# Performance work log

Measured on AMD Instinct MI355X. Metric: run time of the kernel, lower is better.

Reference implementation:

```python
import jax, jax.numpy as jnp
import numpy as np

B, L, C, D = 32, 4096, 64, 128
TOPK = max(1, int(L * 0.5))


def setup_inputs() -> dict:
    key = jax.random.key(0)
    ks = jax.random.split(key, 9)
    s = lambda k, sh: jax.random.normal(k, sh, dtype=jnp.float32) * 0.02
    return {
        "x": jax.random.normal(ks[0], (B, L, C), dtype=jnp.float32),
        "score_w": s(ks[1], (C,)),
        "score_b": jnp.zeros((), jnp.float32),
        "sparse_w": s(ks[2], (C, D)),
        "sparse_b": jnp.zeros((D,), jnp.float32),
        "full_w": s(ks[3], (C, D)),
        "full_b": jnp.zeros((D,), jnp.float32),
        "ln_g": jnp.ones((D,), jnp.float32),
        "ln_b": jnp.zeros((D,), jnp.float32),
    }


def _layernorm(h, g, b, eps=1e-5):
    mu = jnp.mean(h, axis=-1, keepdims=True)
    var = jnp.mean(jnp.square(h - mu), axis=-1, keepdims=True)
    return (h - mu) * jax.lax.rsqrt(var + eps) * g + b


def reference(x, score_w, score_b, sparse_w, sparse_b, full_w, full_b, ln_g, ln_b):
    # scores: (B, L)
    scores = jnp.einsum("blc,c->bl", x, score_w) + score_b
    _, idx = jax.lax.top_k(scores, TOPK)              # (B, K)
    sparse_x = jnp.take_along_axis(x, idx[:, :, None], axis=1)  # (B, K, C)
    sparse_feat = jax.nn.gelu(jnp.einsum("bkc,cd->bkd", sparse_x, sparse_w) + sparse_b, approximate=False)
    sparse_agg = jnp.mean(sparse_feat, axis=1, keepdims=True)   # (B, 1, D)
    full_feat = jnp.einsum("blc,cd->bld", x, full_w) + full_b   # (B, L, D)
    out = _layernorm(full_feat + sparse_agg, ln_g, ln_b)
    return out
```

## Files before the change

### kernel.cpp

```cpp
#include <hip/hip_runtime.h>
#include <math.h>

static constexpr int PB = 32;
static constexpr int PL = 4096;
static constexpr int PC = 64;
static constexpr int PD = 128;
static constexpr int PK = 2048;

typedef __attribute__((ext_vector_type(8))) short bf16x8;
typedef __attribute__((ext_vector_type(4))) float f32x4;

#define MFMA_BF16(A, B, C) __builtin_amdgcn_mfma_f32_16x16x32_bf16(A, B, C, 0, 0, 0)

__device__ inline short f2bf(float f) {
  unsigned u = __float_as_uint(f);
  u += 0x7FFFu + ((u >> 16) & 1u);
  return (short)(u >> 16);
}

__global__ __launch_bounds__(256) void scores_kernel(
    const float* __restrict__ x, const float* __restrict__ score_w,
    const float* __restrict__ score_b, const float* __restrict__ sparse_w,
    const float* __restrict__ full_w, float* __restrict__ scores,
    short* __restrict__ xbf, unsigned* __restrict__ wtfg) {
  int tid = threadIdx.x;

  if (blockIdx.x < 2) {
    const float* w = (blockIdx.x == 0) ? sparse_w : full_w;
    unsigned* dst = wtfg + blockIdx.x * 4096;
    for (int i = tid; i < 4096; i += 256) {
      int d = i & 127, cp = i >> 7, c = cp * 2;
      float va = w[(size_t)c * PD + d];
      float vb = w[(size_t)(c + 1) * PD + d];
      unsigned lo = (unsigned short)f2bf(va);
      unsigned hi = (unsigned short)f2bf(vb);
      int t = d >> 4, dl = d & 15, h = c >> 5, cq = (c >> 3) & 3, jp = (c & 7) >> 1;
      dst[(((t * 2 + h) * 4 + cq) * 16 + dl) * 4 + jp] = lo | (hi << 16);
    }
  }

  int r  = tid >> 4;
  int c4 = tid & 15;
  int row = blockIdx.x * 16 + r;
  float4 xv = *(const float4*)(x + (size_t)row * PC + c4 * 4);
  float4 wv = *(const float4*)(score_w + c4 * 4);

  short4 xbv;
  xbv.x = f2bf(xv.x); xbv.y = f2bf(xv.y); xbv.z = f2bf(xv.z); xbv.w = f2bf(xv.w);
  *(short4*)(xbf + (size_t)row * PC + c4 * 4) = xbv;

  float v = xv.x * wv.x + xv.y * wv.y + xv.z * wv.z + xv.w * wv.w;
  #pragma unroll
  for (int off = 1; off < 16; off <<= 1) v += __shfl_xor(v, off);
  if (c4 == 0) scores[row] = v + score_b[0];
}

__global__ __launch_bounds__(256) void select_kernel(
    const float* __restrict__ scores, int* __restrict__ selidx,
    float* __restrict__ agg) {
  __shared__ unsigned hist4[4 * 256];
  __shared__ unsigned sbuf[257];
  __shared__ unsigned wsum[4];
  __shared__ unsigned sh_prefix, sh_need;

  int tid = threadIdx.x;
  int lane = tid & 63;
  int wid  = tid >> 6;
  int b = blockIdx.x;
  const float* sc = scores + (size_t)b * PL;

  unsigned k[16];
  #pragma unroll
  for (int q = 0; q < 4; ++q) {
    float4 f = *(const float4*)(sc + tid * 16 + q * 4);
    unsigned u0 = __float_as_uint(f.x), u1 = __float_as_uint(f.y);
    unsigned u2 = __float_as_uint(f.z), u3 = __float_as_uint(f.w);
    k[q * 4 + 0] = (u0 & 0x80000000u) ? ~u0 : (u0 | 0x80000000u);
    k[q * 4 + 1] = (u1 & 0x80000000u) ? ~u1 : (u1 | 0x80000000u);
    k[q * 4 + 2] = (u2 & 0x80000000u) ? ~u2 : (u2 | 0x80000000u);
    k[q * 4 + 3] = (u3 & 0x80000000u) ? ~u3 : (u3 | 0x80000000u);
  }

  if (tid == 0) { sh_prefix = 0u; sh_need = (unsigned)PK; sbuf[256] = 0u; }
  if (tid < PD) agg[(size_t)b * PD + tid] = 0.f;

  for (int r = 3; r >= 0; --r) {
    int shift = r * 8;
    #pragma unroll
    for (int w = 0; w < 4; ++w) hist4[w * 256 + tid] = 0u;
    __syncthreads();
    unsigned prefix = sh_prefix;
    unsigned need   = sh_need;
    unsigned maskAbove = (r == 3) ? 0u : (~0u << (shift + 8));
    unsigned* myhist = &hist4[wid * 256];
    #pragma unroll
    for (int j = 0; j < 16; ++j) {
      if ((k[j] & maskAbove) == prefix)
        atomicAdd(&myhist[(k[j] >> shift) & 255u], 1u);
    }
    __syncthreads();
    unsigned v = hist4[tid] + hist4[256 + tid] + hist4[512 + tid] + hist4[768 + tid];
    #pragma unroll
    for (int off = 1; off < 64; off <<= 1) {
      unsigned t = __shfl_down(v, off);
      if (lane + off < 64) v += t;
    }
    if (lane == 0) wsum[wid] = v;
    __syncthreads();
    unsigned add = 0;
    #pragma unroll
    for (int w = 0; w < 4; ++w) if (w > wid) add += wsum[w];
    sbuf[tid] = v + add;
    __syncthreads();
    if (sbuf[tid] >= need && sbuf[tid + 1] < need) {
      sh_prefix = prefix | ((unsigned)tid << shift);
      sh_need = need - sbuf[tid + 1];
    }
  }
  __syncthreads();
  unsigned T = sh_prefix;
  unsigned needEq = sh_need;

  int base = tid * 16;
  unsigned ceq = 0;
  #pragma unroll
  for (int j = 0; j < 16; ++j) ceq += (k[j] == T);

  unsigned v1 = ceq;
  #pragma unroll
  for (int off = 1; off < 64; off <<= 1) {
    unsigned t = __shfl_up(v1, off);
    if (lane >= off) v1 += t;
  }
  if (lane == 63) wsum[wid] = v1;
  __syncthreads();
  unsigned add1 = 0;
  #pragma unroll
  for (int w = 0; w < 4; ++w) if (w < wid) add1 += wsum[w];
  unsigned eqbase = v1 + add1 - ceq;
  __syncthreads();

  unsigned csel = 0, eqr = eqbase;
  #pragma unroll
  for (int j = 0; j < 16; ++j) {
    if (k[j] > T) csel++;
    else if (k[j] == T) { if (eqr < needEq) csel++; eqr++; }
  }
  unsigned v2 = csel;
  #pragma unroll
  for (int off = 1; off < 64; off <<= 1) {
    unsigned t = __shfl_up(v2, off);
    if (lane >= off) v2 += t;
  }
  if (lane == 63) wsum[wid] = v2;
  __syncthreads();
  unsigned add2 = 0;
  #pragma unroll
  for (int w = 0; w < 4; ++w) if (w < wid) add2 += wsum[w];
  unsigned pos = v2 + add2 - csel;

  eqr = eqbase;
  int* outp = selidx + (size_t)b * PK;
  #pragma unroll
  for (int j = 0; j < 16; ++j) {
    bool sel;
    if (k[j] > T) sel = true;
    else if (k[j] == T) { sel = (eqr < needEq); eqr++; }
    else sel = false;
    if (sel) outp[pos++] = base + j;
  }
}

__device__ inline void stage_wtf(const unsigned* __restrict__ g, unsigned* lds, int tid) {
  #pragma unroll
  for (int q = 0; q < 4; ++q) {
    uint4 v = *(const uint4*)(g + q * 1024 + tid * 4);
    *(uint4*)(lds + q * 1024 + tid * 4) = v;
  }
}

__global__ __launch_bounds__(256, 3) void sparse_kernel(
    const short* __restrict__ xbf, const unsigned* __restrict__ wtfg,
    const float* __restrict__ sparse_b, const int* __restrict__ selidx,
    float* __restrict__ agg) {
  __shared__ unsigned WTf[4096];
  __shared__ float red[PD];
  int tid = threadIdx.x;
  stage_wtf(wtfg, WTf, tid);
  if (tid < PD) red[tid] = 0.f;
  __syncthreads();

  int lane = tid & 63, wid = tid >> 6;
  int ln = lane & 15, quad = lane >> 4;
  int b  = blockIdx.x >> 4;
  int rb = blockIdx.x & 15;
  int j0 = rb * 128 + wid * 32 + ln;
  const int* sel = selidx + (size_t)b * PK;
  int r0 = sel[j0], r1 = sel[j0 + 16];

  const short* xb = xbf + (size_t)b * PL * PC;
  const short* p0 = xb + (size_t)r0 * PC + quad * 8;
  const short* p1 = xb + (size_t)r1 * PC + quad * 8;
  bf16x8 a00 = *(const bf16x8*)p0, a01 = *(const bf16x8*)(p0 + 32);
  bf16x8 a10 = *(const bf16x8*)p1, a11 = *(const bf16x8*)(p1 + 32);

  f32x4 acc0[8], acc1[8];
  #pragma unroll
  for (int t = 0; t < 8; ++t) { acc0[t] = (f32x4){0.f,0.f,0.f,0.f}; acc1[t] = (f32x4){0.f,0.f,0.f,0.f}; }

  const short* wb = (const short*)WTf + lane * 8;
  #pragma unroll
  for (int t = 0; t < 8; ++t) {
    bf16x8 b0 = *(const bf16x8*)(wb + (2 * t) * 512);
    bf16x8 b1 = *(const bf16x8*)(wb + (2 * t + 1) * 512);
    acc0[t] = MFMA_BF16(a00, b0, acc0[t]);
    acc0[t] = MFMA_BF16(a01, b1, acc0[t]);
    acc1[t] = MFMA_BF16(a10, b0, acc1[t]);
    acc1[t] = MFMA_BF16(a11, b1, acc1[t]);
  }

  #pragma unroll
  for (int t = 0; t < 8; ++t) {
    float bias = sparse_b[t * 16 + ln];
    float s = 0.f;
    #pragma unroll
    for (int i = 0; i < 4; ++i) {
      float v0 = acc0[t][i] + bias;
      s += 0.5f * v0 * (1.0f + erff(v0 * 0.70710678118654752f));
      float v1 = acc1[t][i] + bias;
      s += 0.5f * v1 * (1.0f + erff(v1 * 0.70710678118654752f));
    }
    s += __shfl_xor(s, 16);
    s += __shfl_xor(s, 32);
    if (quad == 0) atomicAdd(&red[t * 16 + ln], s);
  }
  __syncthreads();
  if (tid < PD) atomicAdd(&agg[(size_t)b * PD + tid], red[tid]);
}

__global__ __launch_bounds__(256, 3) void full_ln_kernel(
    const short* __restrict__ xbf, const unsigned* __restrict__ wtfg,
    const float* __restrict__ full_b, const float* __restrict__ ln_g,
    const float* __restrict__ ln_b, const float* __restrict__ agg,
    float* __restrict__ out) {
  __shared__ unsigned WTf[4096];
  int tid = threadIdx.x;
  stage_wtf(wtfg, WTf, tid);
  __syncthreads();

  int lane = tid & 63, wid = tid >> 6;
  int ln = lane & 15, quad = lane >> 4;
  int rowbase = blockIdx.x * 128 + wid * 32;
  int b = rowbase >> 12;

  const float invK = 1.0f / (float)PK;
  float bias[8], gg[8], bb[8];
  #pragma unroll
  for (int t = 0; t < 8; ++t) {
    int d = t * 16 + ln;
    bias[t] = full_b[d] + agg[(size_t)b * PD + d] * invK;
    gg[t] = ln_g[d];
    bb[t] = ln_b[d];
  }

  const short* p0 = xbf + (size_t)(rowbase + ln) * PC + quad * 8;
  const short* p1 = xbf + (size_t)(rowbase + 16 + ln) * PC + quad * 8;
  bf16x8 a00 = *(const bf16x8*)p0, a01 = *(const bf16x8*)(p0 + 32);
  bf16x8 a10 = *(const bf16x8*)p1, a11 = *(const bf16x8*)(p1 + 32);

  f32x4 acc0[8], acc1[8];
  #pragma unroll
  for (int t = 0; t < 8; ++t) { acc0[t] = (f32x4){0.f,0.f,0.f,0.f}; acc1[t] = (f32x4){0.f,0.f,0.f,0.f}; }

  const short* wb = (const short*)WTf + lane * 8;
  #pragma unroll
  for (int t = 0; t < 8; ++t) {
    bf16x8 b0 = *(const bf16x8*)(wb + (2 * t) * 512);
    bf16x8 b1 = *(const bf16x8*)(wb + (2 * t + 1) * 512);
    acc0[t] = MFMA_BF16(a00, b0, acc0[t]);
    acc0[t] = MFMA_BF16(a01, b1, acc0[t]);
    acc1[t] = MFMA_BF16(a10, b0, acc1[t]);
    acc1[t] = MFMA_BF16(a11, b1, acc1[t]);
  }

#define LN_EPILOGUE(ACC, GOFF) do {                                          \
    float s_[4] = {0.f,0.f,0.f,0.f}, ss_[4] = {0.f,0.f,0.f,0.f};             \
    _Pragma("unroll")                                                        \
    for (int t = 0; t < 8; ++t) {                                            \
      _Pragma("unroll")                                                      \
      for (int i = 0; i < 4; ++i) {                                          \
        float h_ = ACC[t][i] + bias[t];                                      \
        ACC[t][i] = h_;                                                      \
        s_[i] += h_; ss_[i] += h_ * h_;                                      \
      }                                                                      \
    }                                                                        \
    _Pragma("unroll")                                                        \
    for (int i = 0; i < 4; ++i) {                                            \
      _Pragma("unroll")                                                      \
      for (int off = 1; off < 16; off <<= 1) {                               \
        s_[i]  += __shfl_xor(s_[i], off);                                    \
        ss_[i] += __shfl_xor(ss_[i], off);                                   \
      }                                                                      \
    }                                                                        \
    _Pragma("unroll")                                                        \
    for (int i = 0; i < 4; ++i) {                                            \
      float mu_  = s_[i] * (1.0f / 128.0f);                                  \
      float var_ = ss_[i] * (1.0f / 128.0f) - mu_ * mu_;                     \
      float inv_ = rsqrtf(var_ + 1e-5f);                                     \
      int r_ = rowbase + (GOFF) + quad * 4 + i;                              \
      float* op_ = out + (size_t)r_ * PD + ln;                               \
      _Pragma("unroll")                                                      \
      for (int t = 0; t < 8; ++t)                                            \
        op_[t * 16] = (ACC[t][i] - mu_) * inv_ * gg[t] + bb[t];              \
    }                                                                        \
  } while (0)

  LN_EPILOGUE(acc0, 0);
  LN_EPILOGUE(acc1, 16);
#undef LN_EPILOGUE
}

extern "C" void kernel_launch(void* const* d_in, const int* in_sizes, int n_in,
                              void* d_out, int out_size, void* d_ws, size_t ws_size,
                              hipStream_t stream) {
  const float* x        = (const float*)d_in[0];
  const float* score_w  = (const float*)d_in[1];
  const float* score_b  = (const float*)d_in[2];
  const float* sparse_w = (const float*)d_in[3];
  const float* sparse_b = (const float*)d_in[4];
  const float* full_w   = (const float*)d_in[5];
  const float* full_b   = (const float*)d_in[6];
  const float* ln_g     = (const float*)d_in[7];
  const float* ln_b     = (const float*)d_in[8];
  float* out = (float*)d_out;

  char* ws = (char*)d_ws;
  float*    scores = (float*)ws;
  int*      selidx = (int*)(ws + (512 << 10));
  float*    agg    = (float*)(ws + (768 << 10));
  unsigned* wtfg   = (unsigned*)(ws + (784 << 10));
  short*    xbf    = (short*)(ws + (816 << 10));

  scores_kernel<<<PB * PL / 16, 256, 0, stream>>>(x, score_w, score_b, sparse_w,
                                                  full_w, scores, xbf, wtfg);
  select_kernel<<<PB, 256, 0, stream>>>(scores, selidx, agg);
  sparse_kernel<<<PB * (PK / 128), 256, 0, stream>>>(xbf, wtfg, sparse_b, selidx, agg);
  full_ln_kernel<<<PB * PL / 128, 256, 0, stream>>>(xbf, wtfg + 4096, full_b,
                                                    ln_g, ln_b, agg, out);
}
```

Baseline: 131.8 us.

## Fuse score computation and top-k selection via last-block-done atomic counter

Merges the scores kernel and the select kernel into one launch. Each block now processes 128 rows, and the last block to finish for each batch runs the radix-select, detected through a per-batch atomic counter that a memset zeroes before launch. The histogram rows are padded to a stride of 264 to reduce LDS bank conflicts. This removes one kernel launch and its gap, but adds a memset, threadfences, and a serialized select tail inside the fused kernel.

```diff
diff --git a/kernel.cpp b/kernel.cpp
--- a/kernel.cpp
+++ b/kernel.cpp
@@ -12,22 +12,34 @@
 
 #define MFMA_BF16(A, B, C) __builtin_amdgcn_mfma_f32_16x16x32_bf16(A, B, C, 0, 0, 0)
 
+static constexpr int HSTR = 264;
+
 __device__ inline short f2bf(float f) {
   unsigned u = __float_as_uint(f);
   u += 0x7FFFu + ((u >> 16) & 1u);
   return (short)(u >> 16);
 }
 
-__global__ __launch_bounds__(256) void scores_kernel(
+__global__ __launch_bounds__(256) void scores_select_kernel(
     const float* __restrict__ x, const float* __restrict__ score_w,
     const float* __restrict__ score_b, const float* __restrict__ sparse_w,
     const float* __restrict__ full_w, float* __restrict__ scores,
-    short* __restrict__ xbf, unsigned* __restrict__ wtfg) {
+    short* __restrict__ xbf, unsigned* __restrict__ wtfg,
+    int* __restrict__ selidx, float* __restrict__ agg,
+    unsigned* __restrict__ done) {
+  __shared__ unsigned hist4[4 * HSTR];
+  __shared__ unsigned sbuf[257];
+  __shared__ unsigned wsum[4];
+  __shared__ unsigned sh_prefix, sh_need;
+  __shared__ int sh_last;
+
   int tid = threadIdx.x;
-
-  if (blockIdx.x < 2) {
-    const float* w = (blockIdx.x == 0) ? sparse_w : full_w;
-    unsigned* dst = wtfg + blockIdx.x * 4096;
+  int blk = blockIdx.x;
+  int b = blk >> 5;
+
+  if (blk < 2) {
+    const float* w = (blk == 0) ? sparse_w : full_w;
+    unsigned* dst = wtfg + blk * 4096;
     for (int i = tid; i < 4096; i += 256) {
       int d = i & 127, cp = i >> 7, c = cp * 2;
       float va = w[(size_t)c * PD + d];
@@ -41,32 +53,29 @@
 
   int r  = tid >> 4;
   int c4 = tid & 15;
-  int row = blockIdx.x * 16 + r;
-  float4 xv = *(const float4*)(x + (size_t)row * PC + c4 * 4);
   float4 wv = *(const float4*)(score_w + c4 * 4);
-
-  short4 xbv;
-  xbv.x = f2bf(xv.x); xbv.y = f2bf(xv.y); xbv.z = f2bf(xv.z); xbv.w = f2bf(xv.w);
-  *(short4*)(xbf + (size_t)row * PC + c4 * 4) = xbv;
-
-  float v = xv.x * wv.x + xv.y * wv.y + xv.z * wv.z + xv.w * wv.w;
-  #pragma unroll
-  for (int off = 1; off < 16; off <<= 1) v += __shfl_xor(v, off);
-  if (c4 == 0) scores[row] = v + score_b[0];
-}
-
-__global__ __launch_bounds__(256) void select_kernel(
-    const float* __restrict__ scores, int* __restrict__ selidx,
-    float* __restrict__ agg) {
-  __shared__ unsigned hist4[4 * 256];
-  __shared__ unsigned sbuf[257];
-  __shared__ unsigned wsum[4];
-  __shared__ unsigned sh_prefix, sh_need;
-
-  int tid = threadIdx.x;
+  float sb0 = score_b[0];
+  #pragma unroll
+  for (int it = 0; it < 8; ++it) {
+    int row = blk * 128 + it * 16 + r;
+    float4 xv = *(const float4*)(x + (size_t)row * PC + c4 * 4);
+    short4 xbv;
+    xbv.x = f2bf(xv.x); xbv.y = f2bf(xv.y); xbv.z = f2bf(xv.z); xbv.w = f2bf(xv.w);
+    *(short4*)(xbf + (size_t)row * PC + c4 * 4) = xbv;
+    float v = xv.x * wv.x + xv.y * wv.y + xv.z * wv.z + xv.w * wv.w;
+    #pragma unroll
+    for (int off = 1; off < 16; off <<= 1) v += __shfl_xor(v, off);
+    if (c4 == 0) scores[row] = v + sb0;
+  }
+
+  __threadfence();
+  if (tid == 0) sh_last = (atomicAdd(&done[b], 1u) == 31u);
+  __syncthreads();
+  if (!sh_last) return;
+  __threadfence();
+
   int lane = tid & 63;
   int wid  = tid >> 6;
-  int b = blockIdx.x;
   const float* sc = scores + (size_t)b * PL;
 
   unsigned k[16];
@@ -84,22 +93,22 @@
   if (tid == 0) { sh_prefix = 0u; sh_need = (unsigned)PK; sbuf[256] = 0u; }
   if (tid < PD) agg[(size_t)b * PD + tid] = 0.f;
 
-  for (int r = 3; r >= 0; --r) {
-    int shift = r * 8;
-    #pragma unroll
-    for (int w = 0; w < 4; ++w) hist4[w * 256 + tid] = 0u;
+  for (int rr = 3; rr >= 0; --rr) {
+    int shift = rr * 8;
+    #pragma unroll
+    for (int w = 0; w < 4; ++w) hist4[w * HSTR + tid] = 0u;
     __syncthreads();
     unsigned prefix = sh_prefix;
     unsigned need   = sh_need;
-    unsigned maskAbove = (r == 3) ? 0u : (~0u << (shift + 8));
-    unsigned* myhist = &hist4[wid * 256];
+    unsigned maskAbove = (rr == 3) ? 0u : (~0u << (shift + 8));
+    unsigned* myhist = &hist4[wid * HSTR];
     #pragma unroll
     for (int j = 0; j < 16; ++j) {
       if ((k[j] & maskAbove) == prefix)
         atomicAdd(&myhist[(k[j] >> shift) & 255u], 1u);
     }
     __syncthreads();
-    unsigned v = hist4[tid] + hist4[256 + tid] + hist4[512 + tid] + hist4[768 + tid];
+    unsigned v = hist4[tid] + hist4[HSTR + tid] + hist4[2 * HSTR + tid] + hist4[3 * HSTR + tid];
     #pragma unroll
     for (int off = 1; off < 64; off <<= 1) {
       unsigned t = __shfl_down(v, off);
@@ -339,11 +348,12 @@
   int*      selidx = (int*)(ws + (512 << 10));
   float*    agg    = (float*)(ws + (768 << 10));
   unsigned* wtfg   = (unsigned*)(ws + (784 << 10));
-  short*    xbf    = (short*)(ws + (816 << 10));
-
-  scores_kernel<<<PB * PL / 16, 256, 0, stream>>>(x, score_w, score_b, sparse_w,
-                                                  full_w, scores, xbf, wtfg);
-  select_kernel<<<PB, 256, 0, stream>>>(scores, selidx, agg);
+  unsigned* done   = (unsigned*)(ws + (816 << 10));
+  short*    xbf    = (short*)(ws + (817 << 10));
+
+  hipMemsetAsync(done, 0, PB * sizeof(unsigned), stream);
+  scores_select_kernel<<<PB * PL / 128, 256, 0, stream>>>(
+      x, score_w, score_b, sparse_w, full_w, scores, xbf, wtfg, selidx, agg, done);
   sparse_kernel<<<PB * (PK / 128), 256, 0, stream>>>(xbf, wtfg, sparse_b, selidx, agg);
   full_ln_kernel<<<PB * PL / 128, 256, 0, stream>>>(xbf, wtfg + 4096, full_b,
                                                     ln_g, ln_b, agg, out);
```

After: 238.1 us. +80.6%, slower.

## Fuse top-k selection into sparse kernel, recomputing radix select per block

Applied to the files above, without the earlier changes.

Removes the separate select kernel and its selidx global buffer. Each sparse block now redundantly runs the radix top-k threshold search over its batch's 4096 scores and keeps only the 128 selected indices it owns in LDS. The agg zeroing moves into the scores kernel. This saves one launch and the serial 32-block select stage, but the selection work is repeated 16 times per batch and the LDS footprint per block grows.

```diff
diff --git a/kernel.cpp b/kernel.cpp
--- a/kernel.cpp
+++ b/kernel.cpp
@@ -22,7 +22,8 @@
     const float* __restrict__ x, const float* __restrict__ score_w,
     const float* __restrict__ score_b, const float* __restrict__ sparse_w,
     const float* __restrict__ full_w, float* __restrict__ scores,
-    short* __restrict__ xbf, unsigned* __restrict__ wtfg) {
+    short* __restrict__ xbf, unsigned* __restrict__ wtfg,
+    float* __restrict__ agg) {
   int tid = threadIdx.x;
 
   if (blockIdx.x < 2) {
@@ -38,6 +39,8 @@
       dst[(((t * 2 + h) * 4 + cq) * 16 + dl) * 4 + jp] = lo | (hi << 16);
     }
   }
+  if ((blockIdx.x & 255) == 0 && tid < PD)
+    agg[(size_t)(blockIdx.x >> 8) * PD + tid] = 0.f;
 
   int r  = tid >> 4;
   int c4 = tid & 15;
@@ -55,18 +58,33 @@
   if (c4 == 0) scores[row] = v + score_b[0];
 }
 
-__global__ __launch_bounds__(256) void select_kernel(
-    const float* __restrict__ scores, int* __restrict__ selidx,
+__device__ inline void stage_wtf(const unsigned* __restrict__ g, unsigned* lds, int tid) {
+  #pragma unroll
+  for (int q = 0; q < 4; ++q) {
+    uint4 v = *(const uint4*)(g + q * 1024 + tid * 4);
+    *(uint4*)(lds + q * 1024 + tid * 4) = v;
+  }
+}
+
+__global__ __launch_bounds__(256, 3) void sparse_kernel(
+    const short* __restrict__ xbf, const unsigned* __restrict__ wtfg,
+    const float* __restrict__ sparse_b, const float* __restrict__ scores,
     float* __restrict__ agg) {
+  __shared__ unsigned WTf[4096];
+  __shared__ float red[PD];
   __shared__ unsigned hist4[4 * 256];
   __shared__ unsigned sbuf[257];
   __shared__ unsigned wsum[4];
   __shared__ unsigned sh_prefix, sh_need;
+  __shared__ int sel_l[128];
 
   int tid = threadIdx.x;
-  int lane = tid & 63;
-  int wid  = tid >> 6;
-  int b = blockIdx.x;
+  stage_wtf(wtfg, WTf, tid);
+  if (tid < PD) red[tid] = 0.f;
+
+  int lane = tid & 63, wid = tid >> 6;
+  int b  = blockIdx.x >> 4;
+  int rb = blockIdx.x & 15;
   const float* sc = scores + (size_t)b * PL;
 
   unsigned k[16];
@@ -80,18 +98,16 @@
     k[q * 4 + 2] = (u2 & 0x80000000u) ? ~u2 : (u2 | 0x80000000u);
     k[q * 4 + 3] = (u3 & 0x80000000u) ? ~u3 : (u3 | 0x80000000u);
   }
-
   if (tid == 0) { sh_prefix = 0u; sh_need = (unsigned)PK; sbuf[256] = 0u; }
-  if (tid < PD) agg[(size_t)b * PD + tid] = 0.f;
-
-  for (int r = 3; r >= 0; --r) {
-    int shift = r * 8;
+
+  for (int rr = 3; rr >= 0; --rr) {
+    int shift = rr * 8;
     #pragma unroll
     for (int w = 0; w < 4; ++w) hist4[w * 256 + tid] = 0u;
     __syncthreads();
     unsigned prefix = sh_prefix;
     unsigned need   = sh_need;
-    unsigned maskAbove = (r == 3) ? 0u : (~0u << (shift + 8));
+    unsigned maskAbove = (rr == 3) ? 0u : (~0u << (shift + 8));
     unsigned* myhist = &hist4[wid * 256];
     #pragma unroll
     for (int j = 0; j < 16; ++j) {
@@ -159,44 +175,24 @@
   for (int w = 0; w < 4; ++w) if (w < wid) add2 += wsum[w];
   unsigned pos = v2 + add2 - csel;
 
+  int lo = rb * 128;
   eqr = eqbase;
-  int* outp = selidx + (size_t)b * PK;
   #pragma unroll
   for (int j = 0; j < 16; ++j) {
     bool sel;
     if (k[j] > T) sel = true;
     else if (k[j] == T) { sel = (eqr < needEq); eqr++; }
     else sel = false;
-    if (sel) outp[pos++] = base + j;
-  }
-}
-
-__device__ inline void stage_wtf(const unsigned* __restrict__ g, unsigned* lds, int tid) {
-  #pragma unroll
-  for (int q = 0; q < 4; ++q) {
-    uint4 v = *(const uint4*)(g + q * 1024 + tid * 4);
-    *(uint4*)(lds + q * 1024 + tid * 4) = v;
-  }
-}
-
-__global__ __launch_bounds__(256, 3) void sparse_kernel(
-    const short* __restrict__ xbf, const unsigned* __restrict__ wtfg,
-    const float* __restrict__ sparse_b, const int* __restrict__ selidx,
-    float* __restrict__ agg) {
-  __shared__ unsigned WTf[4096];
-  __shared__ float red[PD];
-  int tid = threadIdx.x;
-  stage_wtf(wtfg, WTf, tid);
-  if (tid < PD) red[tid] = 0.f;
-  __syncthreads();
-
-  int lane = tid & 63, wid = tid >> 6;
+    if (sel) {
+      int p = (int)pos++;
+      if (p >= lo && p < lo + 128) sel_l[p - lo] = base + j;
+    }
+  }
+  __syncthreads();
+
   int ln = lane & 15, quad = lane >> 4;
-  int b  = blockIdx.x >> 4;
-  int rb = blockIdx.x & 15;
-  int j0 = rb * 128 + wid * 32 + ln;
-  const int* sel = selidx + (size_t)b * PK;
-  int r0 = sel[j0], r1 = sel[j0 + 16];
+  int jl = wid * 32 + ln;
+  int r0 = sel_l[jl], r1 = sel_l[jl + 16];
 
   const short* xb = xbf + (size_t)b * PL * PC;
   const short* p0 = xb + (size_t)r0 * PC + quad * 8;
@@ -336,15 +332,13 @@
 
   char* ws = (char*)d_ws;
   float*    scores = (float*)ws;
-  int*      selidx = (int*)(ws + (512 << 10));
-  float*    agg    = (float*)(ws + (768 << 10));
-  unsigned* wtfg   = (unsigned*)(ws + (784 << 10));
-  short*    xbf    = (short*)(ws + (816 << 10));
+  float*    agg    = (float*)(ws + (512 << 10));
+  unsigned* wtfg   = (unsigned*)(ws + (528 << 10));
+  short*    xbf    = (short*)(ws + (560 << 10));
 
   scores_kernel<<<PB * PL / 16, 256, 0, stream>>>(x, score_w, score_b, sparse_w,
-                                                  full_w, scores, xbf, wtfg);
-  select_kernel<<<PB, 256, 0, stream>>>(scores, selidx, agg);
-  sparse_kernel<<<PB * (PK / 128), 256, 0, stream>>>(xbf, wtfg, sparse_b, selidx, agg);
+                                                  full_w, scores, xbf, wtfg, agg);
+  sparse_kernel<<<PB * (PK / 128), 256, 0, stream>>>(xbf, wtfg, sparse_b, scores, agg);
   full_ln_kernel<<<PB * PL / 128, 256, 0, stream>>>(xbf, wtfg + 4096, full_b,
                                                     ln_g, ln_b, agg, out);
 }
```

Result: no change. 132.4 us (median of 2 runs) (+0.4%).
